# Performance work log

Measured on AMD Instinct MI355X. Metric: run time of the kernel, lower is better.

The kernel has to match this reference:

```python
import jax, jax.numpy as jnp
import numpy as np

CIN = 256
WINDOWS = (2, 4, 6)
LN_EPS = 1e-5


def _conv1x1(x, w, b):
    # x: (N,C,H,W), w: (O,C), b: (O,)
    return jnp.einsum('nchw,oc->nohw', x, w) + b[None, :, None, None]


def _pos_encoding(C, H, W):
    # Faithful to SinCosPositionalEncoding2D (incl. its w-major flatten + raw view)
    gw, gh = jnp.meshgrid(jnp.arange(W, dtype=jnp.float32),
                          jnp.arange(H, dtype=jnp.float32), indexing='ij')
    pd = C // 4
    omega = 1.0 / (10000.0 ** (jnp.arange(pd, dtype=jnp.float32) / pd))
    ow = gw.reshape(-1)[:, None] * omega[None, :]
    oh = gh.reshape(-1)[:, None] * omega[None, :]
    pe = jnp.concatenate([jnp.sin(ow), jnp.cos(ow), jnp.sin(oh), jnp.cos(oh)], axis=1)  # (W*H, C)
    return pe.reshape(1, C, H, W)  # raw row-major reinterpret, matching torch .view


def _unfold(x, kh, kw, sh, sw):
    # torch F.unfold semantics: (N,C,H,W) -> (N, C*kh*kw, L), L row-major over (oh, ow)
    N, C, H, W = x.shape
    oh = (H - kh) // sh + 1
    ow = (W - kw) // sw + 1
    ih = (jnp.arange(oh) * sh)[:, None] + jnp.arange(kh)[None, :]  # (oh,kh)
    iw = (jnp.arange(ow) * sw)[:, None] + jnp.arange(kw)[None, :]  # (ow,kw)
    p = x[:, :, ih[:, None, :, None], iw[None, :, None, :]]       # (N,C,oh,ow,kh,kw)
    return jnp.transpose(p, (0, 1, 4, 5, 2, 3)).reshape(N, C * kh * kw, oh * ow)


def _fold(p, H, W, kh, kw, sh, sw):
    # torch F.fold semantics: overlap-add scatter back to (N,C,H,W)
    N = p.shape[0]
    C = p.shape[1] // (kh * kw)
    oh = (H - kh) // sh + 1
    ow = (W - kw) // sw + 1
    p = jnp.transpose(p.reshape(N, C, kh, kw, oh, ow), (0, 1, 4, 5, 2, 3))  # (N,C,oh,ow,kh,kw)
    ih = (jnp.arange(oh) * sh)[:, None] + jnp.arange(kh)[None, :]
    iw = (jnp.arange(ow) * sw)[:, None] + jnp.arange(kw)[None, :]
    out = jnp.zeros((N, C, H, W), p.dtype)
    return out.at[:, :, ih[:, None, :, None], iw[None, :, None, :]].add(p)


def _psa(x, ch_wv_w, ch_wv_b, ch_wq_w, ch_wq_b, ch_wz_w, ch_wz_b, ln_g, ln_b,
         sp_wv_w, sp_wv_b, sp_wq_w, sp_wq_b):
    # Polarized Self-Attention (parallel), input (N,C,H',W')
    N, C, Hh, Ww = x.shape
    C2 = C // 2
    HW = Hh * Ww
    # channel-only branch
    wv = _conv1x1(x, ch_wv_w, ch_wv_b).reshape(N, C2, HW)
    wq = jax.nn.softmax(_conv1x1(x, ch_wq_w, ch_wq_b).reshape(N, HW), axis=-1)
    z = jnp.einsum('ncl,nl->nc', wv, wq)                       # (N, C2)
    wz = jnp.einsum('nc,oc->no', z, ch_wz_w) + ch_wz_b         # (N, C)
    m = wz.mean(-1, keepdims=True)
    v = ((wz - m) ** 2).mean(-1, keepdims=True)
    ch_w = jax.nn.sigmoid((wz - m) / jnp.sqrt(v + LN_EPS) * ln_g + ln_b)
    out_ch = x * ch_w[:, :, None, None]
    # spatial-only branch
    sv = _conv1x1(x, sp_wv_w, sp_wv_b).reshape(N, C2, HW)
    sq = jax.nn.softmax(_conv1x1(x, sp_wq_w, sp_wq_b).mean(axis=(2, 3)), axis=-1)  # (N,C2)
    sp_w = jax.nn.sigmoid(jnp.einsum('nc,ncl->nl', sq, sv)).reshape(N, 1, Hh, Ww)
    return out_ch + x * sp_w


def _forward(x, w_exp, b_exp, w_res, b_res, w_fus, b_fus,
             ch_wv_w, ch_wv_b, ch_wq_w, ch_wq_b, ch_wz_w, ch_wz_b, ln_g, ln_b,
             sp_wv_w, sp_wv_b, sp_wq_w, sp_wq_b):
    N, C, H, W = x.shape
    expx = _conv1x1(x, w_exp, b_exp)                 # (N, 3C, H, W)
    branches = jnp.split(expx, len(WINDOWS), axis=1)
    pos = _pos_encoding(C, H, W)
    outs = []
    for i, win in enumerate(WINDOWS):
        sh, sw = H // win, W // win
        kh, kw = sh + H % win, sw + W % win
        K = kh * kw
        u = _unfold(branches[i], kh, kw, sh, sw).reshape(N, C, win * win, K)
        pu = _unfold(pos, kh, kw, sh, sw).reshape(1, C, win * win, K)
        a = _psa(u + pu, ch_wv_w, ch_wv_b, ch_wq_w, ch_wq_b, ch_wz_w, ch_wz_b,
                 ln_g, ln_b, sp_wv_w, sp_wv_b, sp_wq_w, sp_wq_b)
        a = a.reshape(N, C * K, win * win)           # raw view, matching torch
        cnt = _fold(jnp.ones_like(a), H, W, kh, kw, sh, sw)
        f = _fold(a, H, W, kh, kw, sh, sw) / cnt
        outs.append(f)
    out = _conv1x1(jnp.concatenate(outs, axis=1) + expx, w_res, b_res) + x
    return _conv1x1(out, w_fus, b_fus)


def setup_inputs() -> dict:
    key = jax.random.key(0)
    ks = jax.random.split(key, 10)
    C, C2 = CIN, CIN // 2
    s = 0.02
    nrm = lambda k, shp: jax.random.normal(k, shp, jnp.float32) * s
    return {
        'x': jax.random.normal(ks[0], (8, C, 64, 64), jnp.float32),
        'w_exp': nrm(ks[1], (3 * C, C)), 'b_exp': jnp.zeros((3 * C,), jnp.float32),
        'w_res': nrm(ks[2], (C, 3 * C)), 'b_res': jnp.zeros((C,), jnp.float32),
        'w_fus': nrm(ks[3], (C, C)), 'b_fus': jnp.zeros((C,), jnp.float32),
        'ch_wv_w': nrm(ks[4], (C2, C)), 'ch_wv_b': jnp.zeros((C2,), jnp.float32),
        'ch_wq_w': nrm(ks[5], (1, C)), 'ch_wq_b': jnp.zeros((1,), jnp.float32),
        'ch_wz_w': nrm(ks[6], (C, C2)), 'ch_wz_b': jnp.zeros((C,), jnp.float32),
        'ln_g': jnp.ones((C,), jnp.float32), 'ln_b': jnp.zeros((C,), jnp.float32),
        'sp_wv_w': nrm(ks[7], (C2, C)), 'sp_wv_b': jnp.zeros((C2,), jnp.float32),
        'sp_wq_w': nrm(ks[8], (C2, C)), 'sp_wq_b': jnp.zeros((C2,), jnp.float32),
    }


def reference(x, w_exp, b_exp, w_res, b_res, w_fus, b_fus,
              ch_wv_w, ch_wv_b, ch_wq_w, ch_wq_b, ch_wz_w, ch_wz_b, ln_g, ln_b,
              sp_wv_w, sp_wv_b, sp_wq_w, sp_wq_b):
    return _forward(x, w_exp, b_exp, w_res, b_res, w_fus, b_fus,
                    ch_wv_w, ch_wv_b, ch_wq_w, ch_wq_b, ch_wz_w, ch_wz_b, ln_g, ln_b,
                    sp_wv_w, sp_wv_b, sp_wq_w, sp_wq_b)
```

## Files before the change

### kernel.cpp

```cpp
#include <hip/hip_runtime.h>
#include <cstddef>
#include <cstdint>


#define HW 4096
typedef unsigned short ushort_t;
typedef __attribute__((ext_vector_type(8))) short bf16x8;
typedef __attribute__((ext_vector_type(4))) float floatx4;

__device__ __forceinline__ ushort_t f2bf(float f) {
    unsigned u = __float_as_uint(f);
    u += 0x7FFF + ((u >> 16) & 1);
    return (ushort_t)(u >> 16);
}
__device__ __forceinline__ float bf2f(ushort_t h) {
    return __uint_as_float(((unsigned)h) << 16);
}

__device__ __forceinline__ int cnt1f(int y, int sh, int kh, int win) {
    int t = y - kh + sh;
    int lo = t > 0 ? t / sh : 0;
    int hi = min(win - 1, y / sh);
    return hi - lo + 1;
}

__device__ __forceinline__ float posval(int f) {
    int row = f >> 8, col = f & 255;
    int a = row >> 6, b = row & 63;
    int g = col >> 6, k = col & 63;
    float omega = expf(-(float)k * (9.2103403719761836f / 64.f));
    float arg = (g < 2 ? (float)a : (float)b) * omega;
    return (g & 1) ? cosf(arg) : sinf(arg);
}

__device__ __forceinline__ void gload16(const ushort_t* g, ushort_t* l) {
    const __attribute__((address_space(1))) unsigned int* gp =
        reinterpret_cast<const __attribute__((address_space(1))) unsigned int*>(
            reinterpret_cast<uintptr_t>(g));
    __attribute__((address_space(3))) unsigned int* lp =
        reinterpret_cast<__attribute__((address_space(3))) unsigned int*>(
            reinterpret_cast<uintptr_t>(l));
    __builtin_amdgcn_global_load_lds(gp, lp, 16, 0, 0);
}

__global__ __launch_bounds__(256) void prep_all(
    const float* __restrict__ x, const float* __restrict__ W_exp,
    const float* __restrict__ b_exp, const float* __restrict__ wq,
    const float* __restrict__ wq_b, const float* __restrict__ W_fus,
    const float* __restrict__ W_res, const float* __restrict__ b_res,
    const float* __restrict__ b_fus, const float* __restrict__ sp_wq_w,
    const float* __restrict__ ch_wv_w, const float* __restrict__ ch_wz_w,
    float* __restrict__ pos, float* __restrict__ posT,
    ushort_t* __restrict__ xbT, ushort_t* __restrict__ wexpb,
    float* __restrict__ g, float* __restrict__ c0out,
    ushort_t* __restrict__ Wcat, float* __restrict__ biasc,
    float* __restrict__ zeroreg,
    float* __restrict__ W_expT, float* __restrict__ swqT,
    float* __restrict__ chvT, float* __restrict__ chzT,
    float* __restrict__ xpa, float* __restrict__ xp6,
    float* __restrict__ ppa, float* __restrict__ pp6)
{
    __shared__ float smf[1184];
    __shared__ float pr[256];
    __shared__ float pr6[256];
    int b = blockIdx.x, tid = threadIdx.x;
    if (b < 4096) {
        int idx = b * 256 + tid;
        float pv = posval(idx);
        pos[idx] = pv;
        int p2 = idx >> 8, c2 = idx & 255;
        posT[idx] = posval(c2 * 4096 + p2);
        int p = ((b & 15) << 8) + tid;
        int y = p >> 6, xx = p & 63;
        float cf = (float)(cnt1f(y, 10, 14, 6) * cnt1f(xx, 10, 14, 6));
        smf[tid] = pv; smf[256 + tid] = cf * pv;
        __syncthreads();
        for (int s = 128; s > 0; s >>= 1) {
            if (tid < s) { smf[tid] += smf[tid + s]; smf[256 + tid] += smf[256 + tid + s]; }
            __syncthreads();
        }
        if (tid == 0) {
            int slot = (b & 15) * 256 + (b >> 4);
            ppa[slot] = smf[0];
            pp6[slot] = smf[256];
        }
    } else if (b < 12288) {
        int v = b - 4096;
        int p0 = (v & 127) * 32, c0 = ((v >> 7) & 7) * 32, n = v >> 10;
        int cc = tid >> 3, p4 = (tid & 7) * 4;
        const float* src = x + (((size_t)(n * 256 + c0 + cc)) << 12) + p0 + p4;
        float4 vv = *(const float4*)src;
        int pg = p0 + p4;
        int y = pg >> 6, xx = pg & 63;
        float cy = (float)cnt1f(y, 10, 14, 6);
        float s6 = cy * ((float)cnt1f(xx, 10, 14, 6) * vv.x
                       + (float)cnt1f(xx + 1, 10, 14, 6) * vv.y
                       + (float)cnt1f(xx + 2, 10, 14, 6) * vv.z
                       + (float)cnt1f(xx + 3, 10, 14, 6) * vv.w);
        pr[tid] = vv.x + vv.y + vv.z + vv.w;
        pr6[tid] = s6;
        smf[cc * 37 + p4] = vv.x; smf[cc * 37 + p4 + 1] = vv.y;
        smf[cc * 37 + p4 + 2] = vv.z; smf[cc * 37 + p4 + 3] = vv.w;
        __syncthreads();
        int pp = tid >> 3, c4 = (tid & 7) * 4;
        unsigned lo = (unsigned)f2bf(smf[c4 * 37 + pp]) | ((unsigned)f2bf(smf[(c4 + 1) * 37 + pp]) << 16);
        unsigned hi = (unsigned)f2bf(smf[(c4 + 2) * 37 + pp]) | ((unsigned)f2bf(smf[(c4 + 3) * 37 + pp]) << 16);
        *(uint2*)&xbT[(((size_t)(n << 12)) + p0 + pp) * 256 + c0 + c4] = make_uint2(lo, hi);
        if (tid < 32) {
            float s = 0.f, s66 = 0.f;
            #pragma unroll
            for (int k = 0; k < 8; ++k) { s += pr[tid * 8 + k]; s66 += pr6[tid * 8 + k]; }
            int pblk = v & 127;
            xpa[pblk * 2048 + n * 256 + c0 + tid] = s;
            xp6[pblk * 2048 + n * 256 + c0 + tid] = s66;
        }
    } else if (b < 13056) {
        int i = (b - 12288) * 256 + tid;
        wexpb[i] = f2bf(W_exp[i]);
    } else if (b < 13059) {
        int i = b - 13056;
        float* wql = smf;
        float* red = smf + 256;
        wql[tid] = wq[tid];
        red[tid] = wq[tid] * b_exp[i * 256 + tid];
        __syncthreads();
        const float* Wb = W_exp + ((size_t)(i * 256)) * 256 + tid;
        float acc = 0.f;
        #pragma unroll 8
        for (int oc = 0; oc < 256; ++oc) acc = fmaf(wql[oc], Wb[(size_t)oc * 256], acc);
        g[i * 256 + tid] = acc;
        for (int s = 128; s > 0; s >>= 1) { if (tid < s) red[tid] += red[tid + s]; __syncthreads(); }
        if (tid == 0) c0out[i] = red[0] + wq_b[0];
    } else if (b < 13827) {
        int v = b - 13059;
        int o = v & 255, jb = v >> 8;
        float* wrow = smf;
        float* red = smf + 256;
        wrow[tid] = W_fus[o * 256 + tid];
        __syncthreads();
        int j = jb * 256 + tid;
        float acc = 0.f;
        #pragma unroll 8
        for (int c = 0; c < 256; ++c) acc = fmaf(wrow[c], W_res[(size_t)c * 768 + j], acc);
        Wcat[o * 1024 + 256 + j] = f2bf(acc);
        if (jb == 0) {
            Wcat[o * 1024 + tid] = f2bf(wrow[tid]);
            red[tid] = wrow[tid] * b_res[tid];
            __syncthreads();
            for (int s = 128; s > 0; s >>= 1) { if (tid < s) red[tid] += red[tid + s]; __syncthreads(); }
            if (tid == 0) biasc[o] = red[0] + b_fus[o];
        }
    } else if (b < 13875) {
        int i = (b - 13827) * 256 + tid;
        zeroreg[i] = 0.f;
    } else if (b < 14643) {
        int idx = (b - 13875) * 256 + tid;
        W_expT[(idx & 255) * 768 + (idx >> 8)] = W_exp[idx];
    } else if (b < 14771) {
        int idx = (b - 14643) * 256 + tid;
        swqT[(idx & 255) * 128 + (idx >> 8)] = sp_wq_w[idx];
    } else if (b < 14899) {
        int idx = (b - 14771) * 256 + tid;
        chvT[(idx & 255) * 128 + (idx >> 8)] = ch_wv_w[idx];
    } else {
        int idx = (b - 14899) * 256 + tid;
        chzT[(idx & 127) * 256 + (idx >> 7)] = ch_wz_w[idx];
    }
}

__global__ __launch_bounds__(512) void qdot_ubar(
    const float* __restrict__ x, const float* __restrict__ pos,
    const float* __restrict__ g, const float* __restrict__ c0in,
    const float* __restrict__ wq, float* __restrict__ qdot,
    const float* __restrict__ b_exp,
    const float* __restrict__ xpa, const float* __restrict__ xp6,
    const float* __restrict__ ppa, const float* __restrict__ pp6,
    const float* __restrict__ W_expT, float* __restrict__ ubar)
{
    int blk = blockIdx.x, tid = threadIdx.x;
    if (blk < 256) {
        int n = blk >> 5;
        int ph = tid & 127, cq = tid >> 7;
        int p = (blk & 31) * 128 + ph;
        __shared__ float gl[768];
        __shared__ float wql[256];
        __shared__ float4 red4[512];
        for (int k = tid; k < 768; k += 512) gl[k] = g[k];
        if (tid < 256) wql[tid] = wq[tid];
        __syncthreads();
        const float* xp = x + (((size_t)n) << 20) + p;
        const float* pp = pos + p;
        float q0 = 0.f, q1 = 0.f, q2 = 0.f, qp = 0.f;
        #pragma unroll 4
        for (int c = cq * 64; c < cq * 64 + 64; ++c) {
            float xv = xp[(size_t)c << 12];
            float pv = pp[(size_t)c << 12];
            q0 = fmaf(gl[c], xv, q0);
            q1 = fmaf(gl[256 + c], xv, q1);
            q2 = fmaf(gl[512 + c], xv, q2);
            qp = fmaf(wql[c], pv, qp);
        }
        red4[tid] = make_float4(q0, q1, q2, qp);
        __syncthreads();
        if (tid < 128) {
            float4 a = red4[tid], b = red4[128 + tid], cc = red4[256 + tid], d = red4[384 + tid];
            float rp = a.w + b.w + cc.w + d.w;
            qdot[((0 * 8 + n) << 12) + p] = a.x + b.x + cc.x + d.x + rp + c0in[0];
            qdot[((1 * 8 + n) << 12) + p] = a.y + b.y + cc.y + d.y + rp + c0in[1];
            qdot[((2 * 8 + n) << 12) + p] = a.z + b.z + cc.z + d.z + rp + c0in[2];
        }
    } else {
        int v = blk - 256;
        int i = v >> 3, n = v & 7;
        __shared__ float xbl[256];
        if (tid < 256) {
            const float* xp_ = (i < 2) ? xpa : xp6;
            float s = 0.f;
            #pragma unroll 8
            for (int k = 0; k < 128; ++k) s += xp_[k * 2048 + n * 256 + tid];
            xbl[tid] = s;
        }
        __syncthreads();
        if (tid < 256) {
            const float* pp_ = (i < 2) ? ppa : pp6;
            float pb = 0.f;
            #pragma unroll
            for (int k = 0; k < 16; ++k) pb += pp_[k * 256 + tid];
            int win = 2 * (i + 1), sh = 64 / win, kh = sh + 64 % win;
            float Li = (float)(win * win * kh * kh);
            float acc = b_exp[i * 256 + tid] * Li + pb;
            const float* Wc = W_expT + i * 256 + tid;
            #pragma unroll 8
            for (int j = 0; j < 256; ++j) acc = fmaf(Wc[(size_t)j * 768], xbl[j], acc);
            ubar[(i * 8 + n) * 256 + tid] = acc;
        }
    }
}

__global__ __launch_bounds__(256) void pass_b_h(
    const float* __restrict__ qdot, const float* __restrict__ ubar_raw,
    const float* __restrict__ swqT, const float* __restrict__ sp_wq_b,
    const float* __restrict__ sp_wv_w, const float* __restrict__ sp_wv_b,
    const float* __restrict__ W_exp, const float* __restrict__ b_exp,
    float* __restrict__ Mn, float* __restrict__ invZn,
    float* __restrict__ w_eff, float* __restrict__ h, float* __restrict__ btot)
{
    int i = blockIdx.x, n = blockIdx.y, tid = threadIdx.x;
    int b = i * 8 + n;
    int win = 2 * (i + 1), sh = 64 / win, kh = sh + 64 % win;
    float invL = 1.f / (float)(win * win * kh * kh);
    const float* qd = qdot + (((size_t)b) << 12);
    __shared__ float red[256];
    __shared__ float ub[256];
    __shared__ float spq[128];
    __shared__ float we[256];
    float m = -1e30f;
    for (int p = tid; p < HW; p += 256) m = fmaxf(m, qd[p]);
    red[tid] = m; __syncthreads();
    for (int s = 128; s > 0; s >>= 1) { if (tid < s) red[tid] = fmaxf(red[tid], red[tid + s]); __syncthreads(); }
    float M = red[0]; __syncthreads();
    float z = 0.f;
    for (int p = tid; p < HW; p += 256) {
        int y = p >> 6, xx = p & 63;
        float cf = (float)(cnt1f(y, sh, kh, win) * cnt1f(xx, sh, kh, win));
        z += cf * expf(qd[p] - M);
    }
    red[tid] = z; __syncthreads();
    for (int s = 128; s > 0; s >>= 1) { if (tid < s) red[tid] += red[tid + s]; __syncthreads(); }
    float Z = red[0]; __syncthreads();
    if (tid == 0) { Mn[b] = M; invZn[b] = 1.f / Z; }
    ub[tid] = ubar_raw[b * 256 + tid] * invL;
    __syncthreads();
    float sl = -1e30f;
    if (tid < 128) {
        float a = sp_wq_b[tid];
        #pragma unroll 8
        for (int c = 0; c < 256; ++c) a = fmaf(swqT[c * 128 + tid], ub[c], a);
        sl = a;
    }
    red[tid] = sl; __syncthreads();
    for (int s = 128; s > 0; s >>= 1) { if (tid < s) red[tid] = fmaxf(red[tid], red[tid + s]); __syncthreads(); }
    float m2 = red[0]; __syncthreads();
    float e = (tid < 128) ? expf(sl - m2) : 0.f;
    red[tid] = e; __syncthreads();
    for (int s = 128; s > 0; s >>= 1) { if (tid < s) red[tid] += red[tid + s]; __syncthreads(); }
    float S2 = red[0]; __syncthreads();
    if (tid < 128) spq[tid] = e / S2;
    __syncthreads();
    float a = 0.f;
    #pragma unroll 8
    for (int c2 = 0; c2 < 128; ++c2) a = fmaf(spq[c2], sp_wv_w[c2 * 256 + tid], a);
    w_eff[b * 256 + tid] = a;
    we[tid] = a;
    red[tid] = (tid < 128) ? spq[tid] * sp_wv_b[tid] : 0.f;
    __syncthreads();
    for (int s = 128; s > 0; s >>= 1) { if (tid < s) red[tid] += red[tid + s]; __syncthreads(); }
    float beff = red[0]; __syncthreads();
    const float* Wb = W_exp + (size_t)i * 65536 + tid;
    float hacc = 0.f;
    #pragma unroll 8
    for (int oc = 0; oc < 256; ++oc) hacc = fmaf(we[oc], Wb[(size_t)oc * 256], hacc);
    h[b * 256 + tid] = hacc;
    red[tid] = we[tid] * b_exp[i * 256 + tid];
    __syncthreads();
    for (int s = 128; s > 0; s >>= 1) { if (tid < s) red[tid] += red[tid + s]; __syncthreads(); }
    if (tid == 0) btot[b] = red[0] + beff;
}

__global__ __launch_bounds__(512) void spw_t_xq(
    const float* __restrict__ x, const float* __restrict__ pos,
    const float* __restrict__ h, const float* __restrict__ weff,
    const float* __restrict__ qdot, const float* __restrict__ Mn,
    const float* __restrict__ invZn, const float* __restrict__ btot,
    const ushort_t* __restrict__ xbT, const float* __restrict__ posT,
    float* __restrict__ spw, float* __restrict__ xq, float* __restrict__ posq)
{
    int n = blockIdx.y, tid = threadIdx.x;
    int ph = tid & 127, cq = tid >> 7;
    int p0b = blockIdx.x * 128;
    int p = p0b + ph;
    __shared__ float hl[768], wl[768];
    __shared__ float4 red4[512];
    __shared__ float tl[3][128];
    for (int k = tid; k < 768; k += 512) {
        int i = k >> 8, c = k & 255;
        hl[k] = h[(i * 8 + n) * 256 + c];
        wl[k] = weff[(i * 8 + n) * 256 + c];
    }
    __syncthreads();
    const float* xp = x + (((size_t)n) << 20) + p;
    const float* pp = pos + p;
    float a0 = 0.f, a1 = 0.f, a2 = 0.f;
    #pragma unroll 4
    for (int c = cq * 64; c < cq * 64 + 64; ++c) {
        float xv = xp[(size_t)c << 12];
        float pv = pp[(size_t)c << 12];
        a0 += hl[c] * xv + wl[c] * pv;
        a1 += hl[256 + c] * xv + wl[256 + c] * pv;
        a2 += hl[512 + c] * xv + wl[512 + c] * pv;
    }
    red4[tid] = make_float4(a0, a1, a2, 0.f);
    __syncthreads();
    if (tid < 128) {
        float4 aa = red4[tid], bb = red4[128 + tid], cc = red4[256 + tid], dd = red4[384 + tid];
        float av[3] = {aa.x + bb.x + cc.x + dd.x,
                       aa.y + bb.y + cc.y + dd.y,
                       aa.z + bb.z + cc.z + dd.z};
        int y = p >> 6, xx = p & 63;
        #pragma unroll
        for (int i = 0; i < 3; ++i) {
            int b = i * 8 + n;
            int win = 2 * (i + 1), sh = 64 / win, kh = sh + 64 % win;
            float cf = (float)(cnt1f(y, sh, kh, win) * cnt1f(xx, sh, kh, win));
            int idx = (b << 12) + p;
            spw[idx] = 1.f / (1.f + expf(-(av[i] + btot[b])));
            tl[i][ph] = cf * expf(qdot[idx] - Mn[b]) * invZn[b];
        }
    }
    __syncthreads();
    int c = tid & 255;
    int half = tid >> 8;
    float s0 = 0.f, s1 = 0.f, s2 = 0.f;
    if (half == 0) {
        const ushort_t* xb = xbT + (((size_t)((n << 12) + p0b)) << 8) + c;
        #pragma unroll 4
        for (int pl = 0; pl < 128; ++pl) {
            float xv = bf2f(xb[(size_t)pl << 8]);
            s0 = fmaf(tl[0][pl], xv, s0);
            s1 = fmaf(tl[1][pl], xv, s1);
            s2 = fmaf(tl[2][pl], xv, s2);
        }
        atomicAdd(&xq[(0 * 8 + n) * 256 + c], s0);
        atomicAdd(&xq[(1 * 8 + n) * 256 + c], s1);
        atomicAdd(&xq[(2 * 8 + n) * 256 + c], s2);
    } else {
        const float* pt = posT + (((size_t)p0b) << 8) + c;
        #pragma unroll 4
        for (int pl = 0; pl < 128; ++pl) {
            float pv = pt[(size_t)pl << 8];
            s0 = fmaf(tl[0][pl], pv, s0);
            s1 = fmaf(tl[1][pl], pv, s1);
            s2 = fmaf(tl[2][pl], pv, s2);
        }
        atomicAdd(&posq[(0 * 8 + n) * 256 + c], s0);
        atomicAdd(&posq[(1 * 8 + n) * 256 + c], s1);
        atomicAdd(&posq[(2 * 8 + n) * 256 + c], s2);
    }
}

__global__ __launch_bounds__(256) void pass_d_uq(
    const float* __restrict__ W_expT, const float* __restrict__ b_exp,
    const float* __restrict__ xq, const float* __restrict__ posq,
    const float* __restrict__ chvT, const float* __restrict__ ch_wv_b,
    const float* __restrict__ chzT, const float* __restrict__ ch_wz_b,
    const float* __restrict__ ln_g, const float* __restrict__ ln_b,
    float* __restrict__ ch_w)
{
    int i = blockIdx.x, n = blockIdx.y, tid = threadIdx.x;
    int b = i * 8 + n;
    __shared__ float xql[256];
    __shared__ float uql[256];
    __shared__ float zz[128];
    __shared__ float red[256];
    xql[tid] = xq[b * 256 + tid];
    __syncthreads();
    float acc = b_exp[i * 256 + tid] + posq[b * 256 + tid];
    const float* Wc = W_expT + i * 256 + tid;
    #pragma unroll 8
    for (int cin = 0; cin < 256; ++cin) acc = fmaf(Wc[(size_t)cin * 768], xql[cin], acc);
    uql[tid] = acc;
    __syncthreads();
    if (tid < 128) {
        float a = ch_wv_b[tid];
        #pragma unroll 8
        for (int c = 0; c < 256; ++c) a = fmaf(chvT[c * 128 + tid], uql[c], a);
        zz[tid] = a;
    }
    __syncthreads();
    float wz = ch_wz_b[tid];
    #pragma unroll 8
    for (int c2 = 0; c2 < 128; ++c2) wz = fmaf(chzT[c2 * 256 + tid], zz[c2], wz);
    red[tid] = wz; __syncthreads();
    for (int s = 128; s > 0; s >>= 1) { if (tid < s) red[tid] += red[tid + s]; __syncthreads(); }
    float mean = red[0] * (1.f / 256.f); __syncthreads();
    float d = wz - mean;
    red[tid] = d * d; __syncthreads();
    for (int s = 128; s > 0; s >>= 1) { if (tid < s) red[tid] += red[tid + s]; __syncthreads(); }
    float var = red[0] * (1.f / 256.f);
    float xn = d / sqrtf(var + 1e-5f);
    ch_w[b * 256 + tid] = 1.f / (1.f + expf(-(xn * ln_g[tid] + ln_b[tid])));
}

__global__ __launch_bounds__(256) void gemm_expT(
    const ushort_t* __restrict__ Wb, const ushort_t* __restrict__ XT,
    const float* __restrict__ bias, const float* __restrict__ posT,
    const float* __restrict__ chw, const float* __restrict__ spw,
    ushort_t* __restrict__ OutT)
{
    __shared__ __align__(16) ushort_t SM[16384];
    int n = blockIdx.z;
    int p0 = blockIdx.x * 128;
    int o0 = blockIdx.y * 128;
    int t = threadIdx.x;
    int lane = t & 63, wave = t >> 6;
    int wm = (wave & 1) * 64, wn = (wave >> 1) * 64;
    int lr = lane & 15;
    int srow = (wave & 1) * 64 + lane;
    int scol = (wave >> 1) * 8;
    const ushort_t* gA = Wb + (size_t)(o0 + srow) * 256 + scol;
    const ushort_t* gB = XT + (((size_t)(n << 12)) + p0 + srow) * 256 + scol;
    auto stage = [&](int buf, int k0a) {
        ushort_t* base = &SM[buf * 8192 + wave * 512];
        gload16(gA + k0a,      base);
        gload16(gA + k0a + 16, base + 2048);
        gload16(gB + k0a,      base + 4096);
        gload16(gB + k0a + 16, base + 6144);
    };
    floatx4 acc[4][4] = {};
    stage(0, 0);
    __syncthreads();
    int cur = 0;
    for (int k0 = 0; k0 < 256; k0 += 32) {
        if (k0 + 32 < 256) stage(cur ^ 1, k0 + 32);
        int fb = cur * 8192 + ((lane >> 4) << 10);
        bf16x8 af[4], bfr[4];
        #pragma unroll
        for (int mi = 0; mi < 4; ++mi)
            af[mi] = *(const bf16x8*)&SM[fb + (wm + mi * 16 + lr) * 8];
        #pragma unroll
        for (int ni = 0; ni < 4; ++ni)
            bfr[ni] = *(const bf16x8*)&SM[fb + 4096 + (wn + ni * 16 + lr) * 8];
        #pragma unroll
        for (int mi = 0; mi < 4; ++mi)
            #pragma unroll
            for (int ni = 0; ni < 4; ++ni)
                acc[mi][ni] = __builtin_amdgcn_mfma_f32_16x16x32_bf16(
                    af[mi], bfr[ni], acc[mi][ni], 0, 0, 0);
        __syncthreads();
        cur ^= 1;
    }
    int col = lane & 15, rb = (lane >> 4) * 4;
    int ibr = o0 >> 8;
    int bi = ibr * 8 + n;
    #pragma unroll
    for (int r = 0; r < 2; ++r) {
        __syncthreads();
        if (wm == r * 64) {
            #pragma unroll
            for (int mi = 0; mi < 4; ++mi) {
                int o_loc = mi * 16 + rb;
                float4 bo = *(const float4*)&bias[o0 + r * 64 + o_loc];
                #pragma unroll
                for (int ni = 0; ni < 4; ++ni) {
                    int prow = wn + ni * 16 + col;
                    floatx4 v = acc[mi][ni];
                    unsigned lo = (unsigned)f2bf(v[0] + bo.x) | ((unsigned)f2bf(v[1] + bo.y) << 16);
                    unsigned hi = (unsigned)f2bf(v[2] + bo.z) | ((unsigned)f2bf(v[3] + bo.w) << 16);
                    *(uint2*)&SM[prow * 72 + o_loc] = make_uint2(lo, hi);
                }
            }
        }
        __syncthreads();
        #pragma unroll
        for (int it = 0; it < 4; ++it) {
            int slot = it * 256 + t;
            int pl = slot >> 3, j = (slot & 7) * 8;
            uint4 raw = *(const uint4*)&SM[pl * 72 + j];
            float e0 = bf2f((ushort_t)(raw.x & 0xFFFF)), e1 = bf2f((ushort_t)(raw.x >> 16));
            float e2 = bf2f((ushort_t)(raw.y & 0xFFFF)), e3 = bf2f((ushort_t)(raw.y >> 16));
            float e4 = bf2f((ushort_t)(raw.z & 0xFFFF)), e5 = bf2f((ushort_t)(raw.z >> 16));
            float e6 = bf2f((ushort_t)(raw.w & 0xFFFF)), e7 = bf2f((ushort_t)(raw.w >> 16));
            int p = p0 + pl;
            int cbase = (o0 & 255) + r * 64 + j;
            float s = spw[(bi << 12) + p];
            float4 q0 = *(const float4*)&posT[p * 256 + cbase];
            float4 q1 = *(const float4*)&posT[p * 256 + cbase + 4];
            float4 w0 = *(const float4*)&chw[bi * 256 + cbase];
            float4 w1 = *(const float4*)&chw[bi * 256 + cbase + 4];
            float r0 = e0 + (e0 + q0.x) * (w0.x + s);
            float r1 = e1 + (e1 + q0.y) * (w0.y + s);
            float r2 = e2 + (e2 + q0.z) * (w0.z + s);
            float r3 = e3 + (e3 + q0.w) * (w0.w + s);
            float r4 = e4 + (e4 + q1.x) * (w1.x + s);
            float r5 = e5 + (e5 + q1.y) * (w1.y + s);
            float r6 = e6 + (e6 + q1.z) * (w1.z + s);
            float r7 = e7 + (e7 + q1.w) * (w1.w + s);
            uint4 outv;
            outv.x = (unsigned)f2bf(r0) | ((unsigned)f2bf(r1) << 16);
            outv.y = (unsigned)f2bf(r2) | ((unsigned)f2bf(r3) << 16);
            outv.z = (unsigned)f2bf(r4) | ((unsigned)f2bf(r5) << 16);
            outv.w = (unsigned)f2bf(r6) | ((unsigned)f2bf(r7) << 16);
            *(uint4*)&OutT[(((size_t)(n << 12)) + p) * 768 + o0 + r * 64 + j] = outv;
        }
    }
}

__global__ __launch_bounds__(256) void gemm_out(
    const ushort_t* __restrict__ Wcat, const ushort_t* __restrict__ XT,
    const ushort_t* __restrict__ CT, const float* __restrict__ biasc,
    float* __restrict__ Out)
{
    __shared__ __align__(16) ushort_t SM[16384];
    int n = blockIdx.z;
    int p0 = blockIdx.x * 128;
    int o0 = blockIdx.y * 128;
    int t = threadIdx.x;
    int lane = t & 63, wave = t >> 6;
    int wm = (wave & 1) * 64, wn = (wave >> 1) * 64;
    int lr = lane & 15;
    int srow = (wave & 1) * 64 + lane;
    int scol = (wave >> 1) * 8;
    const ushort_t* gA  = Wcat + (size_t)(o0 + srow) * 1024 + scol;
    const ushort_t* gBX = XT + (((size_t)(n << 12)) + p0 + srow) * 256 + scol;
    const ushort_t* gBC = CT + (((size_t)(n << 12)) + p0 + srow) * 768 + scol;
    auto stage = [&](int buf, int k0a) {
        ushort_t* base = &SM[buf * 8192 + wave * 512];
        const ushort_t* pb = (k0a < 256) ? (gBX + k0a) : (gBC + (k0a - 256));
        gload16(gA + k0a,      base);
        gload16(gA + k0a + 16, base + 2048);
        gload16(pb,            base + 4096);
        gload16(pb + 16,       base + 6144);
    };
    floatx4 acc[4][4] = {};
    stage(0, 0);
    __syncthreads();
    int cur = 0;
    for (int k0 = 0; k0 < 1024; k0 += 32) {
        if (k0 + 32 < 1024) stage(cur ^ 1, k0 + 32);
        int fb = cur * 8192 + ((lane >> 4) << 10);
        bf16x8 af[4], bfr[4];
        #pragma unroll
        for (int mi = 0; mi < 4; ++mi)
            af[mi] = *(const bf16x8*)&SM[fb + (wm + mi * 16 + lr) * 8];
        #pragma unroll
        for (int ni = 0; ni < 4; ++ni)
            bfr[ni] = *(const bf16x8*)&SM[fb + 4096 + (wn + ni * 16 + lr) * 8];
        #pragma unroll
        for (int mi = 0; mi < 4; ++mi)
            #pragma unroll
            for (int ni = 0; ni < 4; ++ni)
                acc[mi][ni] = __builtin_amdgcn_mfma_f32_16x16x32_bf16(
                    af[mi], bfr[ni], acc[mi][ni], 0, 0, 0);
        __syncthreads();
        cur ^= 1;
    }
    int col = lane & 15, rb = (lane >> 4) * 4;
    #pragma unroll
    for (int mi = 0; mi < 4; ++mi) {
        int o = o0 + wm + mi * 16 + rb;
        float4 bo = *(const float4*)&biasc[o];
        #pragma unroll
        for (int r = 0; r < 4; ++r) {
            float br = (r == 0) ? bo.x : (r == 1) ? bo.y : (r == 2) ? bo.z : bo.w;
            #pragma unroll
            for (int ni = 0; ni < 4; ++ni) {
                int p = p0 + wn + ni * 16 + col;
                Out[(((size_t)(n * 256 + o + r)) << 12) + p] = acc[mi][ni][r] + br;
            }
        }
    }
}

extern "C" void kernel_launch(void* const* d_in, const int* in_sizes, int n_in,
                              void* d_out, int out_size, void* d_ws, size_t ws_size,
                              hipStream_t stream) {
    const float* x        = (const float*)d_in[0];
    const float* w_exp    = (const float*)d_in[1];
    const float* b_exp    = (const float*)d_in[2];
    const float* w_res    = (const float*)d_in[3];
    const float* b_res    = (const float*)d_in[4];
    const float* w_fus    = (const float*)d_in[5];
    const float* b_fus    = (const float*)d_in[6];
    const float* ch_wv_w  = (const float*)d_in[7];
    const float* ch_wv_b  = (const float*)d_in[8];
    const float* ch_wq_w  = (const float*)d_in[9];
    const float* ch_wq_b  = (const float*)d_in[10];
    const float* ch_wz_w  = (const float*)d_in[11];
    const float* ch_wz_b  = (const float*)d_in[12];
    const float* ln_g     = (const float*)d_in[13];
    const float* ln_b     = (const float*)d_in[14];
    const float* sp_wv_w  = (const float*)d_in[15];
    const float* sp_wv_b  = (const float*)d_in[16];
    const float* sp_wq_w  = (const float*)d_in[17];
    const float* sp_wq_b  = (const float*)d_in[18];
    float* out = (float*)d_out;
    float* ws  = (float*)d_ws;

    float*    pos   = ws + 0;
    float*    posT  = ws + 1048576;
    ushort_t* xbT   = (ushort_t*)(ws + 2097152);
    ushort_t* exT   = (ushort_t*)(ws + 6291456);
    ushort_t* wexpb = (ushort_t*)(ws + 18874368);
    ushort_t* Wcat  = (ushort_t*)(ws + 18972672);
    float*    qdot  = ws + 19103744;
    float*    spw   = ws + 19300352;
    float*    g     = ws + 19398656;
    float*    c0v   = ws + 19399424;
    float*    ubar  = ws + 19399428;
    float*    Mn    = ws + 19410180;
    float*    iZ    = ws + 19410204;
    float*    weff  = ws + 19410228;
    float*    btot  = ws + 19416372;
    float*    hb    = ws + 19416396;
    float*    xq    = ws + 19422540;
    float*    posq  = ws + 19428684;
    float*    chw   = ws + 19434828;
    float*    biasc = ws + 19440972;
    float*    W_expT = ws + 19441228;
    float*    swqT   = ws + 19637836;
    float*    chvT   = ws + 19670604;
    float*    chzT   = ws + 19703372;
    float*    xpa    = ws + 19736140;
    float*    xp6    = ws + 19998284;
    float*    ppa    = ws + 20260428;
    float*    pp6    = ws + 20264524;

    prep_all<<<15027, 256, 0, stream>>>(x, w_exp, b_exp, ch_wq_w, ch_wq_b,
                                        w_fus, w_res, b_res, b_fus,
                                        sp_wq_w, ch_wv_w, ch_wz_w,
                                        pos, posT, xbT, wexpb, g, c0v,
                                        Wcat, biasc, xq,
                                        W_expT, swqT, chvT, chzT,
                                        xpa, xp6, ppa, pp6);
    qdot_ubar<<<280, 512, 0, stream>>>(x, pos, g, c0v, ch_wq_w, qdot,
                                       b_exp, xpa, xp6, ppa, pp6, W_expT, ubar);
    pass_b_h<<<dim3(3, 8), 256, 0, stream>>>(qdot, ubar, swqT, sp_wq_b,
                                             sp_wv_w, sp_wv_b, w_exp, b_exp,
                                             Mn, iZ, weff, hb, btot);
    spw_t_xq<<<dim3(32, 8), 512, 0, stream>>>(x, pos, hb, weff, qdot, Mn, iZ,
                                              btot, xbT, posT, spw, xq, posq);
    pass_d_uq<<<dim3(3, 8), 256, 0, stream>>>(W_expT, b_exp, xq, posq,
                                              chvT, ch_wv_b, chzT, ch_wz_b,
                                              ln_g, ln_b, chw);
    gemm_expT<<<dim3(32, 6, 8), 256, 0, stream>>>(wexpb, xbT, b_exp, posT, chw, spw, exT);
    gemm_out<<<dim3(32, 2, 8), 256, 0, stream>>>(Wcat, xbT, exT, biasc, out);
}
```

Before: 319.1 us.

## Use wave shuffles for reductions, fuse softmax stats, replace LDS-DMA GEMM staging

Block-level shared-memory tree reductions in prep_all become wavefront shuffle reductions. Per-block softmax max and weighted-sum partials are now computed in qdot_ubar, so pass_b_h only merges 32 partials instead of rescanning qdot over 4096 positions with only 24 blocks. Both GEMM kernels drop the double-buffered global_load_lds staging in favor of register loads into padded single-buffered LDS tiles with two barriers per k-step. This removes the async copy overlap and may cost GEMM throughput in exchange for fewer bank conflicts.

```diff
diff --git a/kernel.cpp b/kernel.cpp
--- a/kernel.cpp
+++ b/kernel.cpp
@@ -31,16 +31,6 @@
     float omega = expf(-(float)k * (9.2103403719761836f / 64.f));
     float arg = (g < 2 ? (float)a : (float)b) * omega;
     return (g & 1) ? cosf(arg) : sinf(arg);
-}
-
-__device__ __forceinline__ void gload16(const ushort_t* g, ushort_t* l) {
-    const __attribute__((address_space(1))) unsigned int* gp =
-        reinterpret_cast<const __attribute__((address_space(1))) unsigned int*>(
-            reinterpret_cast<uintptr_t>(g));
-    __attribute__((address_space(3))) unsigned int* lp =
-        reinterpret_cast<__attribute__((address_space(3))) unsigned int*>(
-            reinterpret_cast<uintptr_t>(l));
-    __builtin_amdgcn_global_load_lds(gp, lp, 16, 0, 0);
 }
 
 __global__ __launch_bounds__(256) void prep_all(
@@ -61,8 +51,7 @@
     float* __restrict__ ppa, float* __restrict__ pp6)
 {
     __shared__ float smf[1184];
-    __shared__ float pr[256];
-    __shared__ float pr6[256];
+    __shared__ float wred[8];
     int b = blockIdx.x, tid = threadIdx.x;
     if (b < 4096) {
         int idx = b * 256 + tid;
@@ -73,16 +62,18 @@
         int p = ((b & 15) << 8) + tid;
         int y = p >> 6, xx = p & 63;
         float cf = (float)(cnt1f(y, 10, 14, 6) * cnt1f(xx, 10, 14, 6));
-        smf[tid] = pv; smf[256 + tid] = cf * pv;
-        __syncthreads();
-        for (int s = 128; s > 0; s >>= 1) {
-            if (tid < s) { smf[tid] += smf[tid + s]; smf[256 + tid] += smf[256 + tid + s]; }
-            __syncthreads();
-        }
+        float s1 = pv, s2 = cf * pv;
+        #pragma unroll
+        for (int d = 32; d; d >>= 1) {
+            s1 += __shfl_down(s1, d, 64);
+            s2 += __shfl_down(s2, d, 64);
+        }
+        if ((tid & 63) == 0) { wred[tid >> 6] = s1; wred[4 + (tid >> 6)] = s2; }
+        __syncthreads();
         if (tid == 0) {
             int slot = (b & 15) * 256 + (b >> 4);
-            ppa[slot] = smf[0];
-            pp6[slot] = smf[256];
+            ppa[slot] = wred[0] + wred[1] + wred[2] + wred[3];
+            pp6[slot] = wred[4] + wred[5] + wred[6] + wred[7];
         }
     } else if (b < 12288) {
         int v = b - 4096;
@@ -97,8 +88,17 @@
                        + (float)cnt1f(xx + 1, 10, 14, 6) * vv.y
                        + (float)cnt1f(xx + 2, 10, 14, 6) * vv.z
                        + (float)cnt1f(xx + 3, 10, 14, 6) * vv.w);
-        pr[tid] = vv.x + vv.y + vv.z + vv.w;
-        pr6[tid] = s6;
+        float s = vv.x + vv.y + vv.z + vv.w;
+        #pragma unroll
+        for (int d = 4; d; d >>= 1) {
+            s += __shfl_down(s, d, 8);
+            s6 += __shfl_down(s6, d, 8);
+        }
+        if ((tid & 7) == 0) {
+            int pblk = v & 127;
+            xpa[pblk * 2048 + n * 256 + c0 + cc] = s;
+            xp6[pblk * 2048 + n * 256 + c0 + cc] = s6;
+        }
         smf[cc * 37 + p4] = vv.x; smf[cc * 37 + p4 + 1] = vv.y;
         smf[cc * 37 + p4 + 2] = vv.z; smf[cc * 37 + p4 + 3] = vv.w;
         __syncthreads();
@@ -106,14 +106,6 @@
         unsigned lo = (unsigned)f2bf(smf[c4 * 37 + pp]) | ((unsigned)f2bf(smf[(c4 + 1) * 37 + pp]) << 16);
         unsigned hi = (unsigned)f2bf(smf[(c4 + 2) * 37 + pp]) | ((unsigned)f2bf(smf[(c4 + 3) * 37 + pp]) << 16);
         *(uint2*)&xbT[(((size_t)(n << 12)) + p0 + pp) * 256 + c0 + c4] = make_uint2(lo, hi);
-        if (tid < 32) {
-            float s = 0.f, s66 = 0.f;
-            #pragma unroll
-            for (int k = 0; k < 8; ++k) { s += pr[tid * 8 + k]; s66 += pr6[tid * 8 + k]; }
-            int pblk = v & 127;
-            xpa[pblk * 2048 + n * 256 + c0 + tid] = s;
-            xp6[pblk * 2048 + n * 256 + c0 + tid] = s66;
-        }
     } else if (b < 13056) {
         int i = (b - 12288) * 256 + tid;
         wexpb[i] = f2bf(W_exp[i]);
@@ -175,7 +167,8 @@
     const float* __restrict__ b_exp,
     const float* __restrict__ xpa, const float* __restrict__ xp6,
     const float* __restrict__ ppa, const float* __restrict__ pp6,
-    const float* __restrict__ W_expT, float* __restrict__ ubar)
+    const float* __restrict__ W_expT, float* __restrict__ ubar,
+    float* __restrict__ qpm, float* __restrict__ qpz)
 {
     int blk = blockIdx.x, tid = threadIdx.x;
     if (blk < 256) {
@@ -185,6 +178,7 @@
         __shared__ float gl[768];
         __shared__ float wql[256];
         __shared__ float4 red4[512];
+        __shared__ float pmz[12];
         for (int k = tid; k < 768; k += 512) gl[k] = g[k];
         if (tid < 256) wql[tid] = wq[tid];
         __syncthreads();
@@ -205,9 +199,42 @@
         if (tid < 128) {
             float4 a = red4[tid], b = red4[128 + tid], cc = red4[256 + tid], d = red4[384 + tid];
             float rp = a.w + b.w + cc.w + d.w;
-            qdot[((0 * 8 + n) << 12) + p] = a.x + b.x + cc.x + d.x + rp + c0in[0];
-            qdot[((1 * 8 + n) << 12) + p] = a.y + b.y + cc.y + d.y + rp + c0in[1];
-            qdot[((2 * 8 + n) << 12) + p] = a.z + b.z + cc.z + d.z + rp + c0in[2];
+            float va = a.x + b.x + cc.x + d.x + rp + c0in[0];
+            float vb = a.y + b.y + cc.y + d.y + rp + c0in[1];
+            float vc = a.z + b.z + cc.z + d.z + rp + c0in[2];
+            qdot[((0 * 8 + n) << 12) + p] = va;
+            qdot[((1 * 8 + n) << 12) + p] = vb;
+            qdot[((2 * 8 + n) << 12) + p] = vc;
+            float vv[3] = {va, vb, vc};
+            int y = p >> 6, xx = p & 63;
+            #pragma unroll
+            for (int i = 0; i < 3; ++i) {
+                int win = 2 * (i + 1), sh = 64 / win, kh = sh + 64 % win;
+                float cf = (float)(cnt1f(y, sh, kh, win) * cnt1f(xx, sh, kh, win));
+                float m = vv[i];
+                #pragma unroll
+                for (int d2 = 32; d2; d2 >>= 1) m = fmaxf(m, __shfl_down(m, d2, 64));
+                m = __shfl(m, 0, 64);
+                float z = cf * expf(vv[i] - m);
+                #pragma unroll
+                for (int d2 = 32; d2; d2 >>= 1) z += __shfl_down(z, d2, 64);
+                if ((tid & 63) == 0) {
+                    pmz[i * 4 + (tid >> 6)] = m;
+                    pmz[i * 4 + 2 + (tid >> 6)] = z;
+                }
+            }
+        }
+        __syncthreads();
+        if (tid == 0) {
+            int pb = blk & 31;
+            #pragma unroll
+            for (int i = 0; i < 3; ++i) {
+                float m0 = pmz[i * 4], m1 = pmz[i * 4 + 1];
+                float M = fmaxf(m0, m1);
+                float Z = pmz[i * 4 + 2] * expf(m0 - M) + pmz[i * 4 + 3] * expf(m1 - M);
+                int bidx = (i * 8 + n) * 32 + pb;
+                qpm[bidx] = M; qpz[bidx] = Z;
+            }
         }
     } else {
         int v = blk - 256;
@@ -238,10 +265,11 @@
 }
 
 __global__ __launch_bounds__(256) void pass_b_h(
-    const float* __restrict__ qdot, const float* __restrict__ ubar_raw,
+    const float* __restrict__ ubar_raw,
     const float* __restrict__ swqT, const float* __restrict__ sp_wq_b,
     const float* __restrict__ sp_wv_w, const float* __restrict__ sp_wv_b,
     const float* __restrict__ W_exp, const float* __restrict__ b_exp,
+    const float* __restrict__ qpm, const float* __restrict__ qpz,
     float* __restrict__ Mn, float* __restrict__ invZn,
     float* __restrict__ w_eff, float* __restrict__ h, float* __restrict__ btot)
 {
@@ -249,26 +277,20 @@
     int b = i * 8 + n;
     int win = 2 * (i + 1), sh = 64 / win, kh = sh + 64 % win;
     float invL = 1.f / (float)(win * win * kh * kh);
-    const float* qd = qdot + (((size_t)b) << 12);
     __shared__ float red[256];
     __shared__ float ub[256];
     __shared__ float spq[128];
     __shared__ float we[256];
-    float m = -1e30f;
-    for (int p = tid; p < HW; p += 256) m = fmaxf(m, qd[p]);
-    red[tid] = m; __syncthreads();
-    for (int s = 128; s > 0; s >>= 1) { if (tid < s) red[tid] = fmaxf(red[tid], red[tid + s]); __syncthreads(); }
-    float M = red[0]; __syncthreads();
-    float z = 0.f;
-    for (int p = tid; p < HW; p += 256) {
-        int y = p >> 6, xx = p & 63;
-        float cf = (float)(cnt1f(y, sh, kh, win) * cnt1f(xx, sh, kh, win));
-        z += cf * expf(qd[p] - M);
-    }
-    red[tid] = z; __syncthreads();
-    for (int s = 128; s > 0; s >>= 1) { if (tid < s) red[tid] += red[tid + s]; __syncthreads(); }
-    float Z = red[0]; __syncthreads();
-    if (tid == 0) { Mn[b] = M; invZn[b] = 1.f / Z; }
+    if (tid < 64) {
+        float mm = (tid < 32) ? qpm[b * 32 + tid] : -1e30f;
+        #pragma unroll
+        for (int d = 16; d; d >>= 1) mm = fmaxf(mm, __shfl_down(mm, d, 64));
+        float M = __shfl(mm, 0, 64);
+        float zz = (tid < 32) ? qpz[b * 32 + tid] * expf(qpm[b * 32 + tid] - M) : 0.f;
+        #pragma unroll
+        for (int d = 16; d; d >>= 1) zz += __shfl_down(zz, d, 64);
+        if (tid == 0) { Mn[b] = M; invZn[b] = 1.f / zz; }
+    }
     ub[tid] = ubar_raw[b * 256 + tid] * invL;
     __syncthreads();
     float sl = -1e30f;
@@ -437,47 +459,46 @@
     const float* __restrict__ chw, const float* __restrict__ spw,
     ushort_t* __restrict__ OutT)
 {
-    __shared__ __align__(16) ushort_t SM[16384];
+    __shared__ ushort_t SM[10240];
+    ushort_t* As = SM;
+    ushort_t* Bs = SM + 5120;
     int n = blockIdx.z;
     int p0 = blockIdx.x * 128;
     int o0 = blockIdx.y * 128;
     int t = threadIdx.x;
     int lane = t & 63, wave = t >> 6;
     int wm = (wave & 1) * 64, wn = (wave >> 1) * 64;
-    int lr = lane & 15;
-    int srow = (wave & 1) * 64 + lane;
-    int scol = (wave >> 1) * 8;
-    const ushort_t* gA = Wb + (size_t)(o0 + srow) * 256 + scol;
-    const ushort_t* gB = XT + (((size_t)(n << 12)) + p0 + srow) * 256 + scol;
-    auto stage = [&](int buf, int k0a) {
-        ushort_t* base = &SM[buf * 8192 + wave * 512];
-        gload16(gA + k0a,      base);
-        gload16(gA + k0a + 16, base + 2048);
-        gload16(gB + k0a,      base + 4096);
-        gload16(gB + k0a + 16, base + 6144);
-    };
+    int lr = lane & 15, lk = (lane >> 4) * 8;
+    int ar = t >> 2, ac = (t & 3) * 8;
+    const ushort_t* A0 = Wb + (size_t)(o0 + ar) * 256 + ac;
+    const ushort_t* A1 = Wb + (size_t)(o0 + ar + 64) * 256 + ac;
+    const ushort_t* B0 = XT + (((size_t)(n << 12)) + p0 + ar) * 256 + ac;
+    const ushort_t* B1 = XT + (((size_t)(n << 12)) + p0 + ar + 64) * 256 + ac;
     floatx4 acc[4][4] = {};
-    stage(0, 0);
-    __syncthreads();
-    int cur = 0;
     for (int k0 = 0; k0 < 256; k0 += 32) {
-        if (k0 + 32 < 256) stage(cur ^ 1, k0 + 32);
-        int fb = cur * 8192 + ((lane >> 4) << 10);
+        uint4 a0 = *(const uint4*)(A0 + k0);
+        uint4 a1 = *(const uint4*)(A1 + k0);
+        uint4 b0 = *(const uint4*)(B0 + k0);
+        uint4 b1 = *(const uint4*)(B1 + k0);
+        __syncthreads();
+        *(uint4*)&As[ar * 40 + ac] = a0;
+        *(uint4*)&As[(ar + 64) * 40 + ac] = a1;
+        *(uint4*)&Bs[ar * 40 + ac] = b0;
+        *(uint4*)&Bs[(ar + 64) * 40 + ac] = b1;
+        __syncthreads();
         bf16x8 af[4], bfr[4];
         #pragma unroll
         for (int mi = 0; mi < 4; ++mi)
-            af[mi] = *(const bf16x8*)&SM[fb + (wm + mi * 16 + lr) * 8];
+            af[mi] = *(const bf16x8*)&As[(wm + mi * 16 + lr) * 40 + lk];
         #pragma unroll
         for (int ni = 0; ni < 4; ++ni)
-            bfr[ni] = *(const bf16x8*)&SM[fb + 4096 + (wn + ni * 16 + lr) * 8];
+            bfr[ni] = *(const bf16x8*)&Bs[(wn + ni * 16 + lr) * 40 + lk];
         #pragma unroll
         for (int mi = 0; mi < 4; ++mi)
             #pragma unroll
             for (int ni = 0; ni < 4; ++ni)
                 acc[mi][ni] = __builtin_amdgcn_mfma_f32_16x16x32_bf16(
                     af[mi], bfr[ni], acc[mi][ni], 0, 0, 0);
-        __syncthreads();
-        cur ^= 1;
     }
     int col = lane & 15, rb = (lane >> 4) * 4;
     int ibr = o0 >> 8;
@@ -540,49 +561,49 @@
     const ushort_t* __restrict__ CT, const float* __restrict__ biasc,
     float* __restrict__ Out)
 {
-    __shared__ __align__(16) ushort_t SM[16384];
+    __shared__ ushort_t As[128 * 40];
+    __shared__ ushort_t Bs[128 * 40];
     int n = blockIdx.z;
     int p0 = blockIdx.x * 128;
     int o0 = blockIdx.y * 128;
     int t = threadIdx.x;
     int lane = t & 63, wave = t >> 6;
     int wm = (wave & 1) * 64, wn = (wave >> 1) * 64;
-    int lr = lane & 15;
-    int srow = (wave & 1) * 64 + lane;
-    int scol = (wave >> 1) * 8;
-    const ushort_t* gA  = Wcat + (size_t)(o0 + srow) * 1024 + scol;
-    const ushort_t* gBX = XT + (((size_t)(n << 12)) + p0 + srow) * 256 + scol;
-    const ushort_t* gBC = CT + (((size_t)(n << 12)) + p0 + srow) * 768 + scol;
-    auto stage = [&](int buf, int k0a) {
-        ushort_t* base = &SM[buf * 8192 + wave * 512];
-        const ushort_t* pb = (k0a < 256) ? (gBX + k0a) : (gBC + (k0a - 256));
-        gload16(gA + k0a,      base);
-        gload16(gA + k0a + 16, base + 2048);
-        gload16(pb,            base + 4096);
-        gload16(pb + 16,       base + 6144);
-    };
+    int lr = lane & 15, lk = (lane >> 4) * 8;
+    int ar = t >> 2, ac = (t & 3) * 8;
+    const ushort_t* A0 = Wcat + (size_t)(o0 + ar) * 1024 + ac;
+    const ushort_t* A1 = Wcat + (size_t)(o0 + ar + 64) * 1024 + ac;
+    const ushort_t* BX0 = XT + (((size_t)(n << 12)) + p0 + ar) * 256 + ac;
+    const ushort_t* BX1 = XT + (((size_t)(n << 12)) + p0 + ar + 64) * 256 + ac;
+    const ushort_t* BC0 = CT + (((size_t)(n << 12)) + p0 + ar) * 768 + ac;
+    const ushort_t* BC1 = CT + (((size_t)(n << 12)) + p0 + ar + 64) * 768 + ac;
     floatx4 acc[4][4] = {};
-    stage(0, 0);
-    __syncthreads();
-    int cur = 0;
     for (int k0 = 0; k0 < 1024; k0 += 32) {
-        if (k0 + 32 < 1024) stage(cur ^ 1, k0 + 32);
-        int fb = cur * 8192 + ((lane >> 4) << 10);
+        const ushort_t* pb0 = (k0 < 256) ? (BX0 + k0) : (BC0 + (k0 - 256));
+        const ushort_t* pb1 = (k0 < 256) ? (BX1 + k0) : (BC1 + (k0 - 256));
+        uint4 a0 = *(const uint4*)(A0 + k0);
+        uint4 a1 = *(const uint4*)(A1 + k0);
+        uint4 b0 = *(const uint4*)pb0;
+        uint4 b1 = *(const uint4*)pb1;
+        __syncthreads();
+        *(uint4*)&As[ar * 40 + ac] = a0;
+        *(uint4*)&As[(ar + 64) * 40 + ac] = a1;
+        *(uint4*)&Bs[ar * 40 + ac] = b0;
+        *(uint4*)&Bs[(ar + 64) * 40 + ac] = b1;
+        __syncthreads();
         bf16x8 af[4], bfr[4];
         #pragma unroll
         for (int mi = 0; mi < 4; ++mi)
-            af[mi] = *(const bf16x8*)&SM[fb + (wm + mi * 16 + lr) * 8];
+            af[mi] = *(const bf16x8*)&As[(wm + mi * 16 + lr) * 40 + lk];
         #pragma unroll
         for (int ni = 0; ni < 4; ++ni)
-            bfr[ni] = *(const bf16x8*)&SM[fb + 4096 + (wn + ni * 16 + lr) * 8];
+            bfr[ni] = *(const bf16x8*)&Bs[(wn + ni * 16 + lr) * 40 + lk];
         #pragma unroll
         for (int mi = 0; mi < 4; ++mi)
             #pragma unroll
             for (int ni = 0; ni < 4; ++ni)
                 acc[mi][ni] = __builtin_amdgcn_mfma_f32_16x16x32_bf16(
                     af[mi], bfr[ni], acc[mi][ni], 0, 0, 0);
-        __syncthreads();
-        cur ^= 1;
     }
     int col = lane & 15, rb = (lane >> 4) * 4;
     #pragma unroll
@@ -654,6 +675,8 @@
     float*    xp6    = ws + 19998284;
     float*    ppa    = ws + 20260428;
     float*    pp6    = ws + 20264524;
+    float*    qpm    = ws + 20268620;
+    float*    qpz    = ws + 20269388;
 
     prep_all<<<15027, 256, 0, stream>>>(x, w_exp, b_exp, ch_wq_w, ch_wq_b,
                                         w_fus, w_res, b_res, b_fus,
@@ -663,9 +686,11 @@
                                         W_expT, swqT, chvT, chzT,
                                         xpa, xp6, ppa, pp6);
     qdot_ubar<<<280, 512, 0, stream>>>(x, pos, g, c0v, ch_wq_w, qdot,
-                                       b_exp, xpa, xp6, ppa, pp6, W_expT, ubar);
-    pass_b_h<<<dim3(3, 8), 256, 0, stream>>>(qdot, ubar, swqT, sp_wq_b,
+                                       b_exp, xpa, xp6, ppa, pp6, W_expT, ubar,
+                                       qpm, qpz);
+    pass_b_h<<<dim3(3, 8), 256, 0, stream>>>(ubar, swqT, sp_wq_b,
                                              sp_wv_w, sp_wv_b, w_exp, b_exp,
+                                             qpm, qpz,
                                              Mn, iZ, weff, hb, btot);
     spw_t_xq<<<dim3(32, 8), 512, 0, stream>>>(x, pos, hb, weff, qdot, Mn, iZ,
                                               btot, xbT, posT, spw, xq, posq);
```

Result: faster. 297.8 us (-6.7%).
